# Kernel optimization log

Hardware: AMD Instinct MI355X
Metric: run time of the kernel (lower is better)

The kernel has to match this reference:

```python
import jax, jax.numpy as jnp
import numpy as np

H, D, K = 8, 512, 64
EPS = 1e-12


def _l2norm(x):
    # F.normalize(p=2, dim=-1): x / max(||x||_2, eps)
    n = jnp.sqrt(jnp.sum(x * x, axis=-1, keepdims=True))
    return x / jnp.maximum(n, EPS)


def setup_inputs() -> dict:
    key = jax.random.key(0)
    ks = jax.random.split(key, 8)
    S, B = 1024, 16
    scale = 1.0 / np.sqrt(D)
    return {
        "query": jax.random.normal(ks[0], (S, B, D), dtype=jnp.float32),
        "key": jax.random.normal(ks[1], (S, B, D), dtype=jnp.float32),
        "value": jax.random.normal(ks[2], (S, B, D), dtype=jnp.float32),
        # stacked per-head projection weights, torch Linear convention [out,in]
        "WQ": jax.random.uniform(ks[3], (H, K, D), jnp.float32, -scale, scale),
        "WK": jax.random.uniform(ks[4], (H, K, D), jnp.float32, -scale, scale),
        "WV": jax.random.uniform(ks[5], (H, K, D), jnp.float32, -scale, scale),
        "Wout": jax.random.uniform(ks[6], (D, H * K), jnp.float32,
                                   -1.0 / np.sqrt(H * K), 1.0 / np.sqrt(H * K)),
    }


def reference(query, key, value, WQ, WK, WV, Wout):
    temp = K ** 0.5
    # project all heads at once: [S,B,D] x [H,K,D] -> [B,H,S,K]
    wq = _l2norm(jnp.einsum("sbd,hkd->bhsk", query, WQ))
    wk = _l2norm(jnp.einsum("sbd,hkd->bhsk", key, WK))
    wv = _l2norm(jnp.einsum("sbd,hkd->bhsk", value, WV))
    # cosine-similarity attention scores [B,H,Sq,Sk]
    scores = jnp.einsum("bhsk,bhtk->bhst", wq, wk) / temp
    aff = jax.nn.softmax(scores, axis=-1)
    out = jnp.einsum("bhst,bhtk->bhsk", aff, wv)  # [B,H,S,K]
    # concat heads -> [S,B,H*K] (matches torch per-head concat on last dim)
    Sq, B = query.shape[0], query.shape[1]
    concat = out.transpose(2, 0, 1, 3).reshape(Sq, B, H * K)
    return concat @ Wout.T  # [S,B,D]
```

## Files before the change

### kernel.cpp

```cpp
#include <hip/hip_runtime.h>
#include <cstdint>
#include <cstddef>

typedef unsigned int u32;
typedef unsigned short u16;
typedef __attribute__((ext_vector_type(8))) short short8;
typedef __attribute__((ext_vector_type(4))) float f32x4;

#define S_LEN 1024
#define BATCH 16
#define NHEAD 8
#define DMODEL 512
#define KHD 64
#define NROW (S_LEN * BATCH)

__device__ __forceinline__ u16 f2bf(float f) {
    u32 u = __float_as_uint(f);
    return (u16)((u + 0x7fffu + ((u >> 16) & 1u)) >> 16);
}

__device__ __forceinline__ void gl_lds16(const void* g, void* l) {
    __builtin_amdgcn_global_load_lds(
        (const __attribute__((address_space(1))) void*)(uintptr_t)g,
        (__attribute__((address_space(3))) void*)(uintptr_t)l, 16, 0, 0);
}

__global__ __launch_bounds__(256) void wcvt_kernel(
    const float* __restrict__ WQ, const float* __restrict__ WK,
    const float* __restrict__ WV, const float* __restrict__ Wo,
    u16* __restrict__ dst)
{
    const int m = blockIdx.y;
    const float* __restrict__ src = (m == 0) ? WQ : (m == 1) ? WK : (m == 2) ? WV : Wo;
    const int idx = (blockIdx.x * 256 + threadIdx.x) * 4;
    const float4 v = *(const float4*)(src + idx);
    u16 r[4];
    r[0] = f2bf(v.x); r[1] = f2bf(v.y); r[2] = f2bf(v.z); r[3] = f2bf(v.w);
    *(uint2*)(dst + (size_t)m * DMODEL * DMODEL + idx) = *(uint2*)r;
}

template<int M>
__global__ __launch_bounds__(256) void gemm_kernel(
    const float* __restrict__ A0, const float* __restrict__ A1,
    const u16* __restrict__ Wb,
    u16* __restrict__ outN,
    float* __restrict__ outP)
{
    __shared__ __align__(16) u16 Alds[128 * 72];
    __shared__ __align__(16) u16 Blds[128 * 64];

    const int tid  = threadIdx.x;
    const int wave = tid >> 6;
    const int lane = tid & 63;
    const int m16  = lane & 15;
    const int quad = lane >> 4;
    const int wm   = wave >> 1;
    const int wn   = wave & 1;
    const int n0   = blockIdx.y * 128;
    const int i0   = (M == 2) ? 0 : blockIdx.x * 128;
    const int s0   = (M == 2) ? blockIdx.x * 128 : 0;
    const int bb   = (M == 2) ? blockIdx.z : 0;
    const int z    = (M == 1) ? blockIdx.z : 0;

    const float* __restrict__ A = (M == 1 && z == 1) ? A1 : A0;
    const u16*   __restrict__ B = Wb + ((M == 1) ? (size_t)z * DMODEL * DMODEL : 0);

    f32x4 acc[4][4] = {};

    const int ar = tid >> 1;
    const int ac = (tid & 1) * 32;
    const int brow   = lane >> 3;
    const int bchunk = (lane & 7) ^ (brow & 7);

    for (int kt = 0; kt < DMODEL; kt += 64) {
        float4 av[8];
        const size_t aoff = (M == 2) ? (((size_t)(s0 + ar) * BATCH + bb) * DMODEL)
                                     : ((size_t)(i0 + ar) * DMODEL);
        const float4* ap = (const float4*)(A + aoff + kt + ac);
#pragma unroll
        for (int j = 0; j < 8; j++) av[j] = ap[j];

        __syncthreads();

        {
            const u16* bp = B + ((size_t)(n0 + wave * 32 + brow) * DMODEL + kt) + bchunk * 8;
            u16* lp = &Blds[(wave * 32) * 64];
#pragma unroll
            for (int j = 0; j < 4; j++)
                gl_lds16(bp + (size_t)j * 8 * DMODEL, lp + j * 8 * 64);
        }

#pragma unroll
        for (int g = 0; g < 4; g++) {
            short8 sv;
            const float4 x0 = av[2 * g], x1 = av[2 * g + 1];
            sv[0] = (short)f2bf(x0.x); sv[1] = (short)f2bf(x0.y);
            sv[2] = (short)f2bf(x0.z); sv[3] = (short)f2bf(x0.w);
            sv[4] = (short)f2bf(x1.x); sv[5] = (short)f2bf(x1.y);
            sv[6] = (short)f2bf(x1.z); sv[7] = (short)f2bf(x1.w);
            *(short8*)&Alds[ar * 72 + ac + g * 8] = sv;
        }

        __syncthreads();

#pragma unroll
        for (int half = 0; half < 2; half++) {
            short8 af[4], bfr[4];
#pragma unroll
            for (int mt = 0; mt < 4; mt++)
                af[mt] = *(const short8*)&Alds[(wm * 64 + mt * 16 + m16) * 72 + half * 32 + quad * 8];
#pragma unroll
            for (int nt = 0; nt < 4; nt++)
                bfr[nt] = *(const short8*)&Blds[(wn * 64 + nt * 16 + m16) * 64 +
                                                (((half << 2) + quad) ^ (m16 & 7)) * 8];
#pragma unroll
            for (int mt = 0; mt < 4; mt++)
#pragma unroll
                for (int nt = 0; nt < 4; nt++)
                    acc[mt][nt] = __builtin_amdgcn_mfma_f32_16x16x32_bf16(af[mt], bfr[nt], acc[mt][nt], 0, 0, 0);
        }
    }

    if (M == 1) {
        const int h = (n0 >> 6) + wn;
        u16* outZ = outN + (size_t)z * BATCH * NHEAD * S_LEN * KHD;
#pragma unroll
        for (int mt = 0; mt < 4; mt++) {
#pragma unroll
            for (int r = 0; r < 4; r++) {
                float ss = 0.0f;
#pragma unroll
                for (int nt = 0; nt < 4; nt++) ss += acc[mt][nt][r] * acc[mt][nt][r];
                ss += __shfl_xor(ss, 1);
                ss += __shfl_xor(ss, 2);
                ss += __shfl_xor(ss, 4);
                ss += __shfl_xor(ss, 8);
                const float sc = 1.0f / fmaxf(sqrtf(ss), 1e-12f);
                const int i = i0 + wm * 64 + mt * 16 + quad * 4 + r;
                const int s = i >> 4, b = i & 15;
                u16* op = outZ + (((size_t)b * NHEAD + h) * S_LEN + s) * KHD;
#pragma unroll
                for (int nt = 0; nt < 4; nt++)
                    op[nt * 16 + m16] = f2bf(acc[mt][nt][r] * sc);
            }
        }
    } else if (M == 2) {
        const int h = (n0 >> 6) + wn;
#pragma unroll
        for (int mt = 0; mt < 4; mt++) {
            float scl[4];
#pragma unroll
            for (int r = 0; r < 4; r++) {
                float ss = 0.0f;
#pragma unroll
                for (int nt = 0; nt < 4; nt++) ss += acc[mt][nt][r] * acc[mt][nt][r];
                ss += __shfl_xor(ss, 1);
                ss += __shfl_xor(ss, 2);
                ss += __shfl_xor(ss, 4);
                ss += __shfl_xor(ss, 8);
                scl[r] = 1.0f / fmaxf(sqrtf(ss), 1e-12f);
            }
            const int sbase = s0 + wm * 64 + mt * 16 + quad * 4;
#pragma unroll
            for (int nt = 0; nt < 4; nt++) {
                const int vcol = nt * 16 + m16;
                const u32 lo = (u32)f2bf(acc[mt][nt][0] * scl[0]) |
                               ((u32)f2bf(acc[mt][nt][1] * scl[1]) << 16);
                const u32 hi = (u32)f2bf(acc[mt][nt][2] * scl[2]) |
                               ((u32)f2bf(acc[mt][nt][3] * scl[3]) << 16);
                uint2 pk; pk.x = lo; pk.y = hi;
                u16* dp = outN + (((size_t)bb * NHEAD + h) * KHD + vcol) * S_LEN + sbase;
                *(uint2*)dp = pk;
            }
        }
    } else {
#pragma unroll
        for (int mt = 0; mt < 4; mt++) {
#pragma unroll
            for (int r = 0; r < 4; r++) {
                const int i = i0 + wm * 64 + mt * 16 + quad * 4 + r;
                float* op = outP + (size_t)i * DMODEL + n0 + wn * 64;
#pragma unroll
                for (int nt = 0; nt < 4; nt++)
                    op[nt * 16 + m16] = acc[mt][nt][r];
            }
        }
    }
}

__global__ __launch_bounds__(256) void attn_kernel(
    const u16* __restrict__ wq, const u16* __restrict__ wk, const u16* __restrict__ wvT,
    float* __restrict__ concat)
{
    __shared__ __align__(16) u16 Klds[64 * 64];
    __shared__ __align__(16) u16 Vlds[64 * 64];
    __shared__ __align__(16) u16 Plds[4][2][16 * 72];

    const int tid  = threadIdx.x;
    const int wave = tid >> 6;
    const int lane = tid & 63;
    const int m16  = lane & 15;
    const int quad = lane >> 4;
    const int qt   = blockIdx.x;
    const int bh   = blockIdx.y;

    const u16* Qb = wq  + (size_t)bh * S_LEN * KHD;
    const u16* Kb = wk  + (size_t)bh * S_LEN * KHD;
    const u16* Vb = wvT + (size_t)bh * KHD * S_LEN;

    short8 qf[2][2];
#pragma unroll
    for (int qs = 0; qs < 2; qs++) {
        const int qrow = qt * 128 + wave * 32 + qs * 16 + m16;
#pragma unroll
        for (int hf = 0; hf < 2; hf++)
            qf[qs][hf] = *(const short8*)(Qb + (size_t)qrow * KHD + hf * 32 + quad * 8);
    }

    f32x4 o[2][4] = {};
    float lsum[2] = {0.0f, 0.0f};
    const float SC8 = 0.18033688011112042f;

    const int srow   = lane >> 3;
    const int schunk = (lane & 7) ^ srow;

    for (int it = 0; it < S_LEN / 64; it++) {
        const int kt0 = it * 64;
        __syncthreads();
        {
            const int r0 = wave * 8 + srow;
            gl_lds16(Kb + (size_t)(kt0 + r0) * KHD + schunk * 8,        &Klds[(wave * 8) * 64]);
            gl_lds16(Kb + (size_t)(kt0 + r0 + 32) * KHD + schunk * 8,   &Klds[(wave * 8 + 32) * 64]);
            gl_lds16(Vb + (size_t)r0 * S_LEN + kt0 + schunk * 8,        &Vlds[(wave * 8) * 64]);
            gl_lds16(Vb + (size_t)(r0 + 32) * S_LEN + kt0 + schunk * 8, &Vlds[(wave * 8 + 32) * 64]);
        }
        __syncthreads();

        f32x4 sc[2][4];
#pragma unroll
        for (int mt = 0; mt < 4; mt++) {
            short8 kf0 = *(const short8*)&Klds[(mt * 16 + m16) * 64 + ((quad) ^ (m16 & 7)) * 8];
            short8 kf1 = *(const short8*)&Klds[(mt * 16 + m16) * 64 + ((4 + quad) ^ (m16 & 7)) * 8];
#pragma unroll
            for (int qs = 0; qs < 2; qs++) {
                f32x4 c = {};
                c = __builtin_amdgcn_mfma_f32_16x16x32_bf16(kf0, qf[qs][0], c, 0, 0, 0);
                c = __builtin_amdgcn_mfma_f32_16x16x32_bf16(kf1, qf[qs][1], c, 0, 0, 0);
                sc[qs][mt] = c;
            }
        }

#pragma unroll
        for (int qs = 0; qs < 2; qs++) {
#pragma unroll
            for (int mt = 0; mt < 4; mt++) {
                const float p0 = exp2f(sc[qs][mt][0] * SC8);
                const float p1 = exp2f(sc[qs][mt][1] * SC8);
                const float p2 = exp2f(sc[qs][mt][2] * SC8);
                const float p3 = exp2f(sc[qs][mt][3] * SC8);
                lsum[qs] += (p0 + p1) + (p2 + p3);
                uint2 pk;
                pk.x = (u32)f2bf(p0) | ((u32)f2bf(p1) << 16);
                pk.y = (u32)f2bf(p2) | ((u32)f2bf(p3) << 16);
                *(uint2*)&Plds[wave][qs][m16 * 72 + mt * 16 + quad * 4] = pk;
            }
        }

#pragma unroll
        for (int c = 0; c < 2; c++) {
            short8 pb[2];
#pragma unroll
            for (int qs = 0; qs < 2; qs++)
                pb[qs] = *(const short8*)&Plds[wave][qs][m16 * 72 + c * 32 + quad * 8];
#pragma unroll
            for (int vt = 0; vt < 4; vt++) {
                const short8 vf = *(const short8*)&Vlds[(vt * 16 + m16) * 64 +
                                                        (((c << 2) + quad) ^ (m16 & 7)) * 8];
#pragma unroll
                for (int qs = 0; qs < 2; qs++)
                    o[qs][vt] = __builtin_amdgcn_mfma_f32_16x16x32_bf16(vf, pb[qs], o[qs][vt], 0, 0, 0);
            }
        }
    }

#pragma unroll
    for (int qs = 0; qs < 2; qs++) {
        lsum[qs] += __shfl_xor(lsum[qs], 16);
        lsum[qs] += __shfl_xor(lsum[qs], 32);
    }

    const int b = bh >> 3, h = bh & 7;
#pragma unroll
    for (int qs = 0; qs < 2; qs++) {
        const float inv = 1.0f / lsum[qs];
        const int qrow = qt * 128 + wave * 32 + qs * 16 + m16;
        float* cp = concat + ((size_t)qrow * BATCH + b) * (NHEAD * KHD) + h * KHD;
#pragma unroll
        for (int vt = 0; vt < 4; vt++) {
            float4 v4;
            v4.x = o[qs][vt][0] * inv;
            v4.y = o[qs][vt][1] * inv;
            v4.z = o[qs][vt][2] * inv;
            v4.w = o[qs][vt][3] * inv;
            *(float4*)(cp + vt * 16 + quad * 4) = v4;
        }
    }
}

extern "C" void kernel_launch(void* const* d_in, const int* in_sizes, int n_in,
                              void* d_out, int out_size, void* d_ws, size_t ws_size,
                              hipStream_t stream) {
    const float* q    = (const float*)d_in[0];
    const float* k    = (const float*)d_in[1];
    const float* v    = (const float*)d_in[2];
    const float* WQ   = (const float*)d_in[3];
    const float* WK   = (const float*)d_in[4];
    const float* WV   = (const float*)d_in[5];
    const float* Wout = (const float*)d_in[6];
    float* out = (float*)d_out;

    const size_t per = (size_t)BATCH * NHEAD * S_LEN * KHD;
    u16* wsQKV = (u16*)d_ws;
    u16* wsW   = wsQKV + 3 * per;

    wcvt_kernel<<<dim3(256, 4), 256, 0, stream>>>(WQ, WK, WV, Wout, wsW);

    gemm_kernel<1><<<dim3(NROW / 128, DMODEL / 128, 2), 256, 0, stream>>>(
        q, k, wsW, wsQKV, nullptr);

    gemm_kernel<2><<<dim3(S_LEN / 128, DMODEL / 128, BATCH), 256, 0, stream>>>(
        v, nullptr, wsW + (size_t)2 * DMODEL * DMODEL, wsQKV + 2 * per, nullptr);

    attn_kernel<<<dim3(S_LEN / 128, BATCH * NHEAD), 256, 0, stream>>>(
        wsQKV, wsQKV + per, wsQKV + 2 * per, out);

    gemm_kernel<0><<<dim3(NROW / 128, DMODEL / 128, 1), 256, 0, stream>>>(
        out, nullptr, wsW + (size_t)3 * DMODEL * DMODEL, nullptr, out);
}
```

Baseline: 298.2 us.

## Pre-convert activations to bf16, use polynomial exp and MFMA row sums in attention

Query, key and value are now converted to bf16 by a separate pass before the projection GEMMs. This lets the GEMM stream A tiles straight into LDS with swizzled global-to-LDS loads, instead of loading fp32 into registers and converting there. The attention kernel replaces exp2f with a cubic polynomial, which is valid because cosine scores divided by 8 stay in a small range. It truncates probabilities to bf16, computes row sums with an MFMA against a ones vector, and uses 16 query rows per wave with a doubled grid. Attention output is written as bf16 into the output buffer and copied to workspace before the output GEMM. This adds extra conversion kernels and a device copy, and lowers precision in exchange for less ALU work and less memory traffic in the GEMMs.

```diff
diff --git a/kernel.cpp b/kernel.cpp
--- a/kernel.cpp
+++ b/kernel.cpp
@@ -39,14 +39,27 @@
     *(uint2*)(dst + (size_t)m * DMODEL * DMODEL + idx) = *(uint2*)r;
 }
 
+__global__ __launch_bounds__(256) void xcvt_kernel(
+    const float* __restrict__ s0, const float* __restrict__ s1,
+    u16* __restrict__ dst)
+{
+    const float* __restrict__ src = (blockIdx.y == 0) ? s0 : s1;
+    u16* d = dst + (size_t)blockIdx.y * NROW * DMODEL;
+    const int idx = (blockIdx.x * 256 + threadIdx.x) * 4;
+    const float4 v = *(const float4*)(src + idx);
+    u16 r[4];
+    r[0] = f2bf(v.x); r[1] = f2bf(v.y); r[2] = f2bf(v.z); r[3] = f2bf(v.w);
+    *(uint2*)(d + idx) = *(uint2*)r;
+}
+
 template<int M>
 __global__ __launch_bounds__(256) void gemm_kernel(
-    const float* __restrict__ A0, const float* __restrict__ A1,
+    const u16* __restrict__ Abf,
     const u16* __restrict__ Wb,
     u16* __restrict__ outN,
     float* __restrict__ outP)
 {
-    __shared__ __align__(16) u16 Alds[128 * 72];
+    __shared__ __align__(16) u16 Alds[128 * 64];
     __shared__ __align__(16) u16 Blds[128 * 64];
 
     const int tid  = threadIdx.x;
@@ -57,50 +70,32 @@
     const int wm   = wave >> 1;
     const int wn   = wave & 1;
     const int n0   = blockIdx.y * 128;
-    const int i0   = (M == 2) ? 0 : blockIdx.x * 128;
-    const int s0   = (M == 2) ? blockIdx.x * 128 : 0;
+    const int row0 = blockIdx.x * 128;
+    const int z    = (M == 1) ? blockIdx.z : 0;
     const int bb   = (M == 2) ? blockIdx.z : 0;
-    const int z    = (M == 1) ? blockIdx.z : 0;
-
-    const float* __restrict__ A = (M == 1 && z == 1) ? A1 : A0;
-    const u16*   __restrict__ B = Wb + ((M == 1) ? (size_t)z * DMODEL * DMODEL : 0);
+
+    const u16* __restrict__ A = Abf + (size_t)z * NROW * DMODEL + (size_t)bb * DMODEL;
+    const size_t astr = (M == 2) ? (size_t)BATCH * DMODEL : (size_t)DMODEL;
+    const u16* __restrict__ B = Wb + ((M == 1) ? (size_t)z * DMODEL * DMODEL : 0);
 
     f32x4 acc[4][4] = {};
 
-    const int ar = tid >> 1;
-    const int ac = (tid & 1) * 32;
     const int brow   = lane >> 3;
-    const int bchunk = (lane & 7) ^ (brow & 7);
+    const int bchunk = (lane & 7) ^ brow;
 
     for (int kt = 0; kt < DMODEL; kt += 64) {
-        float4 av[8];
-        const size_t aoff = (M == 2) ? (((size_t)(s0 + ar) * BATCH + bb) * DMODEL)
-                                     : ((size_t)(i0 + ar) * DMODEL);
-        const float4* ap = (const float4*)(A + aoff + kt + ac);
-#pragma unroll
-        for (int j = 0; j < 8; j++) av[j] = ap[j];
-
         __syncthreads();
-
         {
-            const u16* bp = B + ((size_t)(n0 + wave * 32 + brow) * DMODEL + kt) + bchunk * 8;
-            u16* lp = &Blds[(wave * 32) * 64];
-#pragma unroll
-            for (int j = 0; j < 4; j++)
-                gl_lds16(bp + (size_t)j * 8 * DMODEL, lp + j * 8 * 64);
-        }
-
-#pragma unroll
-        for (int g = 0; g < 4; g++) {
-            short8 sv;
-            const float4 x0 = av[2 * g], x1 = av[2 * g + 1];
-            sv[0] = (short)f2bf(x0.x); sv[1] = (short)f2bf(x0.y);
-            sv[2] = (short)f2bf(x0.z); sv[3] = (short)f2bf(x0.w);
-            sv[4] = (short)f2bf(x1.x); sv[5] = (short)f2bf(x1.y);
-            sv[6] = (short)f2bf(x1.z); sv[7] = (short)f2bf(x1.w);
-            *(short8*)&Alds[ar * 72 + ac + g * 8] = sv;
-        }
-
+            const u16* ap = A + (size_t)(row0 + wave * 32 + brow) * astr + kt + bchunk * 8;
+            const u16* bp = B + (size_t)(n0 + wave * 32 + brow) * DMODEL + kt + bchunk * 8;
+            u16* la = &Alds[(wave * 32) * 64];
+            u16* lb = &Blds[(wave * 32) * 64];
+#pragma unroll
+            for (int j = 0; j < 4; j++) {
+                gl_lds16(ap + (size_t)j * 8 * astr,   la + j * 8 * 64);
+                gl_lds16(bp + (size_t)j * 8 * DMODEL, lb + j * 8 * 64);
+            }
+        }
         __syncthreads();
 
 #pragma unroll
@@ -108,7 +103,8 @@
             short8 af[4], bfr[4];
 #pragma unroll
             for (int mt = 0; mt < 4; mt++)
-                af[mt] = *(const short8*)&Alds[(wm * 64 + mt * 16 + m16) * 72 + half * 32 + quad * 8];
+                af[mt] = *(const short8*)&Alds[(wm * 64 + mt * 16 + m16) * 64 +
+                                               (((half << 2) + quad) ^ (m16 & 7)) * 8];
 #pragma unroll
             for (int nt = 0; nt < 4; nt++)
                 bfr[nt] = *(const short8*)&Blds[(wn * 64 + nt * 16 + m16) * 64 +
@@ -136,7 +132,7 @@
                 ss += __shfl_xor(ss, 4);
                 ss += __shfl_xor(ss, 8);
                 const float sc = 1.0f / fmaxf(sqrtf(ss), 1e-12f);
-                const int i = i0 + wm * 64 + mt * 16 + quad * 4 + r;
+                const int i = row0 + wm * 64 + mt * 16 + quad * 4 + r;
                 const int s = i >> 4, b = i & 15;
                 u16* op = outZ + (((size_t)b * NHEAD + h) * S_LEN + s) * KHD;
 #pragma unroll
@@ -160,15 +156,15 @@
                 ss += __shfl_xor(ss, 8);
                 scl[r] = 1.0f / fmaxf(sqrtf(ss), 1e-12f);
             }
-            const int sbase = s0 + wm * 64 + mt * 16 + quad * 4;
+            const int sbase = row0 + wm * 64 + mt * 16 + quad * 4;
 #pragma unroll
             for (int nt = 0; nt < 4; nt++) {
                 const int vcol = nt * 16 + m16;
-                const u32 lo = (u32)f2bf(acc[mt][nt][0] * scl[0]) |
-                               ((u32)f2bf(acc[mt][nt][1] * scl[1]) << 16);
-                const u32 hi = (u32)f2bf(acc[mt][nt][2] * scl[2]) |
-                               ((u32)f2bf(acc[mt][nt][3] * scl[3]) << 16);
-                uint2 pk; pk.x = lo; pk.y = hi;
+                uint2 pk;
+                pk.x = (u32)f2bf(acc[mt][nt][0] * scl[0]) |
+                       ((u32)f2bf(acc[mt][nt][1] * scl[1]) << 16);
+                pk.y = (u32)f2bf(acc[mt][nt][2] * scl[2]) |
+                       ((u32)f2bf(acc[mt][nt][3] * scl[3]) << 16);
                 u16* dp = outN + (((size_t)bb * NHEAD + h) * KHD + vcol) * S_LEN + sbase;
                 *(uint2*)dp = pk;
             }
@@ -178,7 +174,7 @@
         for (int mt = 0; mt < 4; mt++) {
 #pragma unroll
             for (int r = 0; r < 4; r++) {
-                const int i = i0 + wm * 64 + mt * 16 + quad * 4 + r;
+                const int i = row0 + wm * 64 + mt * 16 + quad * 4 + r;
                 float* op = outP + (size_t)i * DMODEL + n0 + wn * 64;
 #pragma unroll
                 for (int nt = 0; nt < 4; nt++)
@@ -190,11 +186,11 @@
 
 __global__ __launch_bounds__(256) void attn_kernel(
     const u16* __restrict__ wq, const u16* __restrict__ wk, const u16* __restrict__ wvT,
-    float* __restrict__ concat)
+    u16* __restrict__ Xc)
 {
     __shared__ __align__(16) u16 Klds[64 * 64];
     __shared__ __align__(16) u16 Vlds[64 * 64];
-    __shared__ __align__(16) u16 Plds[4][2][16 * 72];
+    __shared__ __align__(16) u16 Plds[4][16 * 72];
 
     const int tid  = threadIdx.x;
     const int wave = tid >> 6;
@@ -208,18 +204,17 @@
     const u16* Kb = wk  + (size_t)bh * S_LEN * KHD;
     const u16* Vb = wvT + (size_t)bh * KHD * S_LEN;
 
-    short8 qf[2][2];
-#pragma unroll
-    for (int qs = 0; qs < 2; qs++) {
-        const int qrow = qt * 128 + wave * 32 + qs * 16 + m16;
-#pragma unroll
-        for (int hf = 0; hf < 2; hf++)
-            qf[qs][hf] = *(const short8*)(Qb + (size_t)qrow * KHD + hf * 32 + quad * 8);
-    }
-
-    f32x4 o[2][4] = {};
-    float lsum[2] = {0.0f, 0.0f};
-    const float SC8 = 0.18033688011112042f;
+    const int qrow = qt * 64 + wave * 16 + m16;
+    const short8 qf0 = *(const short8*)(Qb + (size_t)qrow * KHD + quad * 8);
+    const short8 qf1 = *(const short8*)(Qb + (size_t)qrow * KHD + 32 + quad * 8);
+
+    short8 ones;
+#pragma unroll
+    for (int j = 0; j < 8; j++) ones[j] = (short)0x3F80;
+
+    f32x4 o[4] = {};
+    f32x4 ls  = {};
+    const float C1 = 0.125f, C2 = 0.0078125f, C3 = 3.2552083e-4f;
 
     const int srow   = lane >> 3;
     const int schunk = (lane & 7) ^ srow;
@@ -236,74 +231,48 @@
         }
         __syncthreads();
 
-        f32x4 sc[2][4];
 #pragma unroll
         for (int mt = 0; mt < 4; mt++) {
-            short8 kf0 = *(const short8*)&Klds[(mt * 16 + m16) * 64 + ((quad) ^ (m16 & 7)) * 8];
-            short8 kf1 = *(const short8*)&Klds[(mt * 16 + m16) * 64 + ((4 + quad) ^ (m16 & 7)) * 8];
-#pragma unroll
-            for (int qs = 0; qs < 2; qs++) {
-                f32x4 c = {};
-                c = __builtin_amdgcn_mfma_f32_16x16x32_bf16(kf0, qf[qs][0], c, 0, 0, 0);
-                c = __builtin_amdgcn_mfma_f32_16x16x32_bf16(kf1, qf[qs][1], c, 0, 0, 0);
-                sc[qs][mt] = c;
-            }
-        }
-
-#pragma unroll
-        for (int qs = 0; qs < 2; qs++) {
-#pragma unroll
-            for (int mt = 0; mt < 4; mt++) {
-                const float p0 = exp2f(sc[qs][mt][0] * SC8);
-                const float p1 = exp2f(sc[qs][mt][1] * SC8);
-                const float p2 = exp2f(sc[qs][mt][2] * SC8);
-                const float p3 = exp2f(sc[qs][mt][3] * SC8);
-                lsum[qs] += (p0 + p1) + (p2 + p3);
-                uint2 pk;
-                pk.x = (u32)f2bf(p0) | ((u32)f2bf(p1) << 16);
-                pk.y = (u32)f2bf(p2) | ((u32)f2bf(p3) << 16);
-                *(uint2*)&Plds[wave][qs][m16 * 72 + mt * 16 + quad * 4] = pk;
-            }
+            const short8 kf0 = *(const short8*)&Klds[(mt * 16 + m16) * 64 + (quad ^ (m16 & 7)) * 8];
+            const short8 kf1 = *(const short8*)&Klds[(mt * 16 + m16) * 64 + ((4 + quad) ^ (m16 & 7)) * 8];
+            f32x4 c = {};
+            c = __builtin_amdgcn_mfma_f32_16x16x32_bf16(kf0, qf0, c, 0, 0, 0);
+            c = __builtin_amdgcn_mfma_f32_16x16x32_bf16(kf1, qf1, c, 0, 0, 0);
+            u32 up[4];
+#pragma unroll
+            for (int r = 0; r < 4; r++) {
+                const float y = c[r];
+                const float p = fmaf(fmaf(fmaf(C3, y, C2), y, C1), y, 1.0f);
+                up[r] = __float_as_uint(p);
+            }
+            uint2 pk;
+            pk.x = (up[0] >> 16) | (up[1] & 0xffff0000u);
+            pk.y = (up[2] >> 16) | (up[3] & 0xffff0000u);
+            *(uint2*)&Plds[wave][m16 * 72 + mt * 16 + quad * 4] = pk;
         }
 
 #pragma unroll
         for (int c = 0; c < 2; c++) {
-            short8 pb[2];
-#pragma unroll
-            for (int qs = 0; qs < 2; qs++)
-                pb[qs] = *(const short8*)&Plds[wave][qs][m16 * 72 + c * 32 + quad * 8];
+            const short8 pb = *(const short8*)&Plds[wave][m16 * 72 + c * 32 + quad * 8];
+            ls = __builtin_amdgcn_mfma_f32_16x16x32_bf16(ones, pb, ls, 0, 0, 0);
 #pragma unroll
             for (int vt = 0; vt < 4; vt++) {
                 const short8 vf = *(const short8*)&Vlds[(vt * 16 + m16) * 64 +
                                                         (((c << 2) + quad) ^ (m16 & 7)) * 8];
-#pragma unroll
-                for (int qs = 0; qs < 2; qs++)
-                    o[qs][vt] = __builtin_amdgcn_mfma_f32_16x16x32_bf16(vf, pb[qs], o[qs][vt], 0, 0, 0);
+                o[vt] = __builtin_amdgcn_mfma_f32_16x16x32_bf16(vf, pb, o[vt], 0, 0, 0);
             }
         }
     }
 
-#pragma unroll
-    for (int qs = 0; qs < 2; qs++) {
-        lsum[qs] += __shfl_xor(lsum[qs], 16);
-        lsum[qs] += __shfl_xor(lsum[qs], 32);
-    }
-
+    const float inv = 1.0f / ls[0];
     const int b = bh >> 3, h = bh & 7;
-#pragma unroll
-    for (int qs = 0; qs < 2; qs++) {
-        const float inv = 1.0f / lsum[qs];
-        const int qrow = qt * 128 + wave * 32 + qs * 16 + m16;
-        float* cp = concat + ((size_t)qrow * BATCH + b) * (NHEAD * KHD) + h * KHD;
-#pragma unroll
-        for (int vt = 0; vt < 4; vt++) {
-            float4 v4;
-            v4.x = o[qs][vt][0] * inv;
-            v4.y = o[qs][vt][1] * inv;
-            v4.z = o[qs][vt][2] * inv;
-            v4.w = o[qs][vt][3] * inv;
-            *(float4*)(cp + vt * 16 + quad * 4) = v4;
-        }
+    u16* cp = Xc + ((size_t)qrow * BATCH + b) * (NHEAD * KHD) + h * KHD;
+#pragma unroll
+    for (int vt = 0; vt < 4; vt++) {
+        uint2 pk;
+        pk.x = (u32)f2bf(o[vt][0] * inv) | ((u32)f2bf(o[vt][1] * inv) << 16);
+        pk.y = (u32)f2bf(o[vt][2] * inv) | ((u32)f2bf(o[vt][3] * inv) << 16);
+        *(uint2*)(cp + vt * 16 + quad * 4) = pk;
     }
 }
 
@@ -318,6 +287,7 @@
     const float* WV   = (const float*)d_in[5];
     const float* Wout = (const float*)d_in[6];
     float* out = (float*)d_out;
+    u16*  Xbf = (u16*)d_out;
 
     const size_t per = (size_t)BATCH * NHEAD * S_LEN * KHD;
     u16* wsQKV = (u16*)d_ws;
@@ -325,15 +295,22 @@
 
     wcvt_kernel<<<dim3(256, 4), 256, 0, stream>>>(WQ, WK, WV, Wout, wsW);
 
+    xcvt_kernel<<<dim3(NROW * DMODEL / 1024, 2), 256, 0, stream>>>(q, k, Xbf);
+
     gemm_kernel<1><<<dim3(NROW / 128, DMODEL / 128, 2), 256, 0, stream>>>(
-        q, k, wsW, wsQKV, nullptr);
+        Xbf, wsW, wsQKV, nullptr);
+
+    xcvt_kernel<<<dim3(NROW * DMODEL / 1024, 1), 256, 0, stream>>>(v, v, Xbf);
 
     gemm_kernel<2><<<dim3(S_LEN / 128, DMODEL / 128, BATCH), 256, 0, stream>>>(
-        v, nullptr, wsW + (size_t)2 * DMODEL * DMODEL, wsQKV + 2 * per, nullptr);
-
-    attn_kernel<<<dim3(S_LEN / 128, BATCH * NHEAD), 256, 0, stream>>>(
-        wsQKV, wsQKV + per, wsQKV + 2 * per, out);
+        Xbf, wsW + (size_t)2 * DMODEL * DMODEL, wsQKV + 2 * per, nullptr);
+
+    attn_kernel<<<dim3(S_LEN / 64, BATCH * NHEAD), 256, 0, stream>>>(
+        wsQKV, wsQKV + per, wsQKV + 2 * per, Xbf);
+
+    hipMemcpyAsync(wsQKV, Xbf, (size_t)NROW * DMODEL * sizeof(u16),
+                   hipMemcpyDeviceToDevice, stream);
 
     gemm_kernel<0><<<dim3(NROW / 128, DMODEL / 128, 1), 256, 0, stream>>>(
-        out, nullptr, wsW + (size_t)3 * DMODEL * DMODEL, nullptr, out);
-}
+        wsQKV, wsW + (size_t)3 * DMODEL * DMODEL, nullptr, out);
+}
```

After: 283.4 us. 1.05x faster.
